# Optimization experiments

Hardware: AMD Instinct MI355X
Metric: run time of the kernel (lower is better)

## Reference

```python
import jax, jax.numpy as jnp
import numpy as np

N_NODES = 20000
N_ANCHORS = 64
D_IN = 128
D_OUT = 128
N_EDGES = N_NODES * N_ANCHORS  # 1,280,000


def setup_inputs() -> dict:
    key = jax.random.key(0)
    ks = jax.random.split(key, 8)
    feature = jax.random.normal(ks[0], (N_NODES, D_IN), dtype=jnp.float32)
    sp_dist = jax.random.uniform(ks[1], (N_EDGES,), dtype=jnp.float32)
    # xavier_uniform with relu gain ~ sqrt(2)*sqrt(6/(fan_in+fan_out))
    def xavier(k, fan_in, fan_out):
        bound = jnp.sqrt(2.0) * jnp.sqrt(6.0 / (fan_in + fan_out))
        return jax.random.uniform(k, (fan_in, fan_out), dtype=jnp.float32,
                                  minval=-bound, maxval=bound)
    Wu = xavier(ks[2], D_IN, D_OUT)
    Wv = xavier(ks[3], D_IN, D_OUT)
    Wpos = xavier(ks[4], D_OUT, 1)
    bu = jnp.zeros((D_OUT,), jnp.float32)
    bv = jnp.zeros((D_OUT,), jnp.float32)
    bpos = jnp.zeros((1,), jnp.float32)
    src = jax.random.randint(ks[5], (N_EDGES,), 0, N_NODES, dtype=jnp.int32)
    dst = jax.random.randint(ks[6], (N_EDGES,), 0, N_NODES, dtype=jnp.int32)
    anchor_eid = jax.random.randint(ks[7], (N_EDGES,), 0, N_EDGES, dtype=jnp.int32)
    return {"feature": feature, "sp_dist": sp_dist, "Wu": Wu, "bu": bu,
            "Wv": Wv, "bv": bv, "Wpos": Wpos, "bpos": bpos,
            "src": src, "dst": dst, "anchor_eid": anchor_eid}


def reference(feature, sp_dist, Wu, bu, Wv, bv, Wpos, bpos, src, dst, anchor_eid):
    # Dense projections of node features (linear_hidden_u / linear_hidden_v)
    u_feat = feature @ Wu + bu  # [N, D_OUT]
    v_feat = feature @ Wv + bv  # [N, D_OUT]
    # apply_edges u_mul_e + v_add_e, then index_select on anchor edges.
    # Gathering at anchor edges directly computes the same values as
    # computing all edge messages and then selecting the anchor subset.
    s = src[anchor_eid]            # [E]
    d = dst[anchor_eid]            # [E]
    sp = sp_dist[anchor_eid]       # [E]
    messages = u_feat[s] * sp[:, None] + v_feat[d]       # [E, D_OUT]
    messages = jax.nn.relu(messages).reshape(N_NODES, N_ANCHORS, D_OUT)
    out_position = (messages @ Wpos + bpos)[..., 0]      # [N, K]
    out_structure = messages.mean(axis=1)                # [N, D_OUT]
    return out_position, out_structure
```

## Files before the change

### kernel.cpp

```cpp
#include <hip/hip_runtime.h>

#define N_NODES   20000
#define N_ANCHORS 64
#define D         128
#define N_EDGES   (N_NODES * N_ANCHORS)
#define NCHUNK    4
#define CDIM      32

typedef float f32x4  __attribute__((ext_vector_type(4)));
typedef short bf16x8 __attribute__((ext_vector_type(8)));

static __device__ __forceinline__ unsigned short f32_to_bf16(float x) {
    unsigned int u = __float_as_uint(x);
    u += 0x7FFFu + ((u >> 16) & 1u);
    return (unsigned short)(u >> 16);
}
static __device__ __forceinline__ float bf_lo(unsigned int w) {
    return __uint_as_float(w << 16);
}
static __device__ __forceinline__ float bf_hi(unsigned int w) {
    return __uint_as_float(w & 0xFFFF0000u);
}

__global__ __launch_bounds__(256) void pack_kernel(
    const int* __restrict__ src, const int* __restrict__ dst,
    const float* __restrict__ sp_dist,
    unsigned long long* __restrict__ epack)
{
    const int e = blockIdx.x * 256 + threadIdx.x;
    const unsigned int s = (unsigned int)__builtin_nontemporal_load(&src[e]);
    const unsigned int d = (unsigned int)__builtin_nontemporal_load(&dst[e]);
    const float       sp = __builtin_nontemporal_load(&sp_dist[e]);
    epack[e] = (unsigned long long)(s | (d << 15)) |
               ((unsigned long long)__float_as_uint(sp) << 32);
}

__global__ __launch_bounds__(256) void meta_kernel(
    const unsigned long long* __restrict__ epack,
    const int* __restrict__ anchor_eid,
    unsigned long long* __restrict__ meta)
{
    const int e = blockIdx.x * 256 + threadIdx.x;
    const int eid = __builtin_nontemporal_load(&anchor_eid[e]);
    const unsigned long long m = epack[eid];
    __builtin_nontemporal_store(m, &meta[e]);
}

__global__ __launch_bounds__(256) void wcvt_kernel(
    const float* __restrict__ Wu, const float* __restrict__ Wv,
    unsigned short* __restrict__ Wt_u, unsigned short* __restrict__ Wt_v)
{
    const int t = blockIdx.x * 256 + threadIdx.x;
    const int k = t >> 7, j = t & 127;
    Wt_u[j * D + k] = f32_to_bf16(Wu[t]);
    Wt_v[j * D + k] = f32_to_bf16(Wv[t]);
}

__global__ __launch_bounds__(256) void proj_mfma_kernel(
    const float* __restrict__ feature,
    const unsigned short* __restrict__ Wt_u,
    const unsigned short* __restrict__ Wt_v,
    const float* __restrict__ bu, const float* __restrict__ bv,
    unsigned short* __restrict__ u_c, unsigned short* __restrict__ v_c)
{
    const int wave = threadIdx.x >> 6;
    const int lane = threadIdx.x & 63;
    const int n0   = blockIdx.x * 16;
    const int mat    = wave & 1;
    const int ctbase = (wave >> 1) * 4;

    const int row = lane & 15;
    const int kq  = lane >> 4;

    bf16x8 afrag[4];
    #pragma unroll
    for (int kt = 0; kt < 4; ++kt) {
        const float* fp = feature + (size_t)(n0 + row) * D + kt * 32 + kq * 8;
        const f32x4 f0 = *(const f32x4*)fp;
        const f32x4 f1 = *(const f32x4*)(fp + 4);
        bf16x8 a;
        #pragma unroll
        for (int e = 0; e < 4; ++e) a[e]     = (short)f32_to_bf16(f0[e]);
        #pragma unroll
        for (int e = 0; e < 4; ++e) a[4 + e] = (short)f32_to_bf16(f1[e]);
        afrag[kt] = a;
    }

    const unsigned short* Wt   = mat ? Wt_v : Wt_u;
    const float*          bias = mat ? bv   : bu;
    unsigned short*       outp = mat ? v_c  : u_c;

    #pragma unroll
    for (int t = 0; t < 4; ++t) {
        const int ct = ctbase + t;
        const int j  = ct * 16 + row;
        f32x4 acc = {0.f, 0.f, 0.f, 0.f};
        #pragma unroll
        for (int kt = 0; kt < 4; ++kt) {
            const bf16x8 b = *(const bf16x8*)(Wt + (size_t)j * D + kt * 32 + kq * 8);
            acc = __builtin_amdgcn_mfma_f32_16x16x32_bf16(afrag[kt], b, acc, 0, 0, 0);
        }
        const float bj  = bias[j];
        const int  cj   = ct >> 1;
        const int  dimc = (ct & 1) * 16 + row;
        #pragma unroll
        for (int r = 0; r < 4; ++r) {
            const int n = n0 + kq * 4 + r;
            outp[((size_t)cj * N_NODES + n) * CDIM + dimc] = f32_to_bf16(acc[r] + bj);
        }
    }
}

__global__ __launch_bounds__(256) void prefill_pos_kernel(
    const float* __restrict__ bpos, float* __restrict__ out_pos)
{
    const int i = blockIdx.x * 256 + threadIdx.x;
    const float bp = bpos[0];
    f32x4 v = {bp, bp, bp, bp};
    __builtin_nontemporal_store(v, (f32x4*)out_pos + i);
}

__global__ __launch_bounds__(256) void fused_chunk_kernel(
    const unsigned short* __restrict__ u_c, const unsigned short* __restrict__ v_c,
    const unsigned long long* __restrict__ meta,
    const float* __restrict__ Wpos,
    float* __restrict__ out_pos, float* __restrict__ out_struct)
{
    const int bid   = blockIdx.x;
    const int x     = bid & 7;
    const int chunk = x >> 1;
    const int half  = x & 1;
    const int nb    = bid >> 3;
    const int wave  = threadIdx.x >> 6;
    const int lane  = threadIdx.x & 63;
    const int n     = half * 10000 + nb * 4 + wave;

    const int sub = lane & 3;
    const int grp = lane >> 2;

    const unsigned long long mm =
        __builtin_nontemporal_load(&meta[(size_t)n * N_ANCHORS + lane]);
    const int   s  = (int)(mm & 0x7FFFu);
    const int   d  = (int)((mm >> 15) & 0x7FFFu);
    const float sp = __uint_as_float((unsigned int)(mm >> 32));

    const float4 wpA = ((const float4*)Wpos)[chunk * 8 + sub * 2];
    const float4 wpB = ((const float4*)Wpos)[chunk * 8 + sub * 2 + 1];

    const unsigned short* ub = u_c + (size_t)chunk * N_NODES * CDIM;
    const unsigned short* vb = v_c + (size_t)chunk * N_NODES * CDIM;

    float acc[8];
    #pragma unroll
    for (int k = 0; k < 8; ++k) acc[k] = 0.f;

    __shared__ float posbuf[4][N_ANCHORS];

    #pragma unroll
    for (int it = 0; it < 4; ++it) {
        const int a = it * 16 + grp;
        const int   sa  = __shfl(s,  a);
        const int   da  = __shfl(d,  a);
        const float spa = __shfl(sp, a);

        const uint4 uu = *(const uint4*)(ub + (size_t)sa * CDIM + sub * 8);
        const uint4 vv = *(const uint4*)(vb + (size_t)da * CDIM + sub * 8);

        float m[8];
        m[0] = fmaf(bf_lo(uu.x), spa, bf_lo(vv.x));
        m[1] = fmaf(bf_hi(uu.x), spa, bf_hi(vv.x));
        m[2] = fmaf(bf_lo(uu.y), spa, bf_lo(vv.y));
        m[3] = fmaf(bf_hi(uu.y), spa, bf_hi(vv.y));
        m[4] = fmaf(bf_lo(uu.z), spa, bf_lo(vv.z));
        m[5] = fmaf(bf_hi(uu.z), spa, bf_hi(vv.z));
        m[6] = fmaf(bf_lo(uu.w), spa, bf_lo(vv.w));
        m[7] = fmaf(bf_hi(uu.w), spa, bf_hi(vv.w));
        #pragma unroll
        for (int k = 0; k < 8; ++k) m[k] = fmaxf(m[k], 0.f);
        #pragma unroll
        for (int k = 0; k < 8; ++k) acc[k] += m[k];

        float p = m[0] * wpA.x + m[1] * wpA.y + m[2] * wpA.z + m[3] * wpA.w
                + m[4] * wpB.x + m[5] * wpB.y + m[6] * wpB.z + m[7] * wpB.w;
        p += __shfl_xor(p, 2);
        p += __shfl_xor(p, 1);
        if (sub == 0) posbuf[wave][a] = p;
    }

    #pragma unroll
    for (int k = 0; k < 8; ++k) {
        acc[k] += __shfl_xor(acc[k], 4);
        acc[k] += __shfl_xor(acc[k], 8);
        acc[k] += __shfl_xor(acc[k], 16);
        acc[k] += __shfl_xor(acc[k], 32);
    }

    __syncthreads();

    atomicAdd(&out_pos[(size_t)n * N_ANCHORS + lane], posbuf[wave][lane]);

    if (grp == 0) {
        const float inv = 1.0f / (float)N_ANCHORS;
        f32x4 o0, o1;
        o0.x = acc[0] * inv; o0.y = acc[1] * inv; o0.z = acc[2] * inv; o0.w = acc[3] * inv;
        o1.x = acc[4] * inv; o1.y = acc[5] * inv; o1.z = acc[6] * inv; o1.w = acc[7] * inv;
        float* os = out_struct + (size_t)n * D + chunk * CDIM + sub * 8;
        __builtin_nontemporal_store(o0, (f32x4*)os);
        __builtin_nontemporal_store(o1, (f32x4*)(os + 4));
    }
}

extern "C" void kernel_launch(void* const* d_in, const int* in_sizes, int n_in,
                              void* d_out, int out_size, void* d_ws, size_t ws_size,
                              hipStream_t stream) {
    const float* feature    = (const float*)d_in[0];
    const float* sp_dist    = (const float*)d_in[1];
    const float* Wu         = (const float*)d_in[2];
    const float* bu         = (const float*)d_in[3];
    const float* Wv         = (const float*)d_in[4];
    const float* bv         = (const float*)d_in[5];
    const float* Wpos       = (const float*)d_in[6];
    const float* bpos       = (const float*)d_in[7];
    const int*   src        = (const int*)d_in[8];
    const int*   dst        = (const int*)d_in[9];
    const int*   anchor_eid = (const int*)d_in[10];

    unsigned short* u_c = (unsigned short*)d_ws;
    unsigned short* v_c = u_c + (size_t)NCHUNK * N_NODES * CDIM;
    unsigned long long* epack = (unsigned long long*)d_ws;
    unsigned long long* meta =
        (unsigned long long*)((char*)d_ws + (size_t)2 * NCHUNK * N_NODES * CDIM * 2);

    float* out_pos    = (float*)d_out;
    float* out_struct = out_pos + (size_t)N_EDGES;

    unsigned short* Wt_u = (unsigned short*)out_struct;
    unsigned short* Wt_v = Wt_u + D * D;

    pack_kernel<<<N_EDGES / 256, 256, 0, stream>>>(src, dst, sp_dist, epack);
    meta_kernel<<<N_EDGES / 256, 256, 0, stream>>>(epack, anchor_eid, meta);
    wcvt_kernel<<<(D * D) / 256, 256, 0, stream>>>(Wu, Wv, Wt_u, Wt_v);
    proj_mfma_kernel<<<N_NODES / 16, 256, 0, stream>>>(feature, Wt_u, Wt_v,
                                                       bu, bv, u_c, v_c);
    prefill_pos_kernel<<<N_EDGES / 1024, 256, 0, stream>>>(bpos, out_pos);
    fused_chunk_kernel<<<N_NODES * NCHUNK / 4, 256, 0, stream>>>(
        u_c, v_c, meta, Wpos, out_pos, out_struct);
}
```

Measured before the change: 126.9 us.

## Merge pack, weight-convert and prefill kernels; use packed float2 math in fused kernel

```diff
diff --git a/kernel.cpp b/kernel.cpp
--- a/kernel.cpp
+++ b/kernel.cpp
@@ -7,6 +7,7 @@
 #define NCHUNK    4
 #define CDIM      32
 
+typedef float f32x2  __attribute__((ext_vector_type(2)));
 typedef float f32x4  __attribute__((ext_vector_type(4)));
 typedef short bf16x8 __attribute__((ext_vector_type(8)));
 
@@ -15,24 +16,44 @@
     u += 0x7FFFu + ((u >> 16) & 1u);
     return (unsigned short)(u >> 16);
 }
-static __device__ __forceinline__ float bf_lo(unsigned int w) {
-    return __uint_as_float(w << 16);
-}
-static __device__ __forceinline__ float bf_hi(unsigned int w) {
-    return __uint_as_float(w & 0xFFFF0000u);
-}
-
-__global__ __launch_bounds__(256) void pack_kernel(
+static __device__ __forceinline__ f32x2 bf2(unsigned int w) {
+    f32x2 r;
+    r.x = __uint_as_float(w << 16);
+    r.y = __uint_as_float(w & 0xFFFF0000u);
+    return r;
+}
+
+#define NB_PACK    (N_EDGES / 256)
+#define NB_WCVT    ((D * D) / 256)
+#define NB_PREFILL (N_EDGES / 1024)
+__global__ __launch_bounds__(256) void prep_kernel(
     const int* __restrict__ src, const int* __restrict__ dst,
     const float* __restrict__ sp_dist,
-    unsigned long long* __restrict__ epack)
-{
-    const int e = blockIdx.x * 256 + threadIdx.x;
-    const unsigned int s = (unsigned int)__builtin_nontemporal_load(&src[e]);
-    const unsigned int d = (unsigned int)__builtin_nontemporal_load(&dst[e]);
-    const float       sp = __builtin_nontemporal_load(&sp_dist[e]);
-    epack[e] = (unsigned long long)(s | (d << 15)) |
-               ((unsigned long long)__float_as_uint(sp) << 32);
+    const float* __restrict__ Wu, const float* __restrict__ Wv,
+    const float* __restrict__ bpos,
+    unsigned long long* __restrict__ epack,
+    unsigned short* __restrict__ Wt_u, unsigned short* __restrict__ Wt_v,
+    float* __restrict__ out_pos)
+{
+    const int bid = blockIdx.x;
+    if (bid < NB_PACK) {
+        const int e = bid * 256 + threadIdx.x;
+        const unsigned int s = (unsigned int)__builtin_nontemporal_load(&src[e]);
+        const unsigned int d = (unsigned int)__builtin_nontemporal_load(&dst[e]);
+        const float       sp = __builtin_nontemporal_load(&sp_dist[e]);
+        epack[e] = (unsigned long long)(s | (d << 15)) |
+                   ((unsigned long long)__float_as_uint(sp) << 32);
+    } else if (bid < NB_PACK + NB_WCVT) {
+        const int t = (bid - NB_PACK) * 256 + threadIdx.x;
+        const int k = t >> 7, j = t & 127;
+        Wt_u[j * D + k] = f32_to_bf16(Wu[t]);
+        Wt_v[j * D + k] = f32_to_bf16(Wv[t]);
+    } else {
+        const int i = (bid - NB_PACK - NB_WCVT) * 256 + threadIdx.x;
+        const float bp = bpos[0];
+        f32x4 v = {bp, bp, bp, bp};
+        __builtin_nontemporal_store(v, (f32x4*)out_pos + i);
+    }
 }
 
 __global__ __launch_bounds__(256) void meta_kernel(
@@ -44,16 +65,6 @@
     const int eid = __builtin_nontemporal_load(&anchor_eid[e]);
     const unsigned long long m = epack[eid];
     __builtin_nontemporal_store(m, &meta[e]);
-}
-
-__global__ __launch_bounds__(256) void wcvt_kernel(
-    const float* __restrict__ Wu, const float* __restrict__ Wv,
-    unsigned short* __restrict__ Wt_u, unsigned short* __restrict__ Wt_v)
-{
-    const int t = blockIdx.x * 256 + threadIdx.x;
-    const int k = t >> 7, j = t & 127;
-    Wt_u[j * D + k] = f32_to_bf16(Wu[t]);
-    Wt_v[j * D + k] = f32_to_bf16(Wv[t]);
 }
 
 __global__ __launch_bounds__(256) void proj_mfma_kernel(
@@ -109,15 +120,6 @@
             outp[((size_t)cj * N_NODES + n) * CDIM + dimc] = f32_to_bf16(acc[r] + bj);
         }
     }
-}
-
-__global__ __launch_bounds__(256) void prefill_pos_kernel(
-    const float* __restrict__ bpos, float* __restrict__ out_pos)
-{
-    const int i = blockIdx.x * 256 + threadIdx.x;
-    const float bp = bpos[0];
-    f32x4 v = {bp, bp, bp, bp};
-    __builtin_nontemporal_store(v, (f32x4*)out_pos + i);
 }
 
 __global__ __launch_bounds__(256) void fused_chunk_kernel(
@@ -144,15 +146,18 @@
     const int   d  = (int)((mm >> 15) & 0x7FFFu);
     const float sp = __uint_as_float((unsigned int)(mm >> 32));
 
-    const float4 wpA = ((const float4*)Wpos)[chunk * 8 + sub * 2];
-    const float4 wpB = ((const float4*)Wpos)[chunk * 8 + sub * 2 + 1];
+    f32x2 wp[4];
+    {
+        const f32x2* wpp = (const f32x2*)(Wpos + chunk * CDIM + sub * 8);
+        #pragma unroll
+        for (int q = 0; q < 4; ++q) wp[q] = wpp[q];
+    }
 
     const unsigned short* ub = u_c + (size_t)chunk * N_NODES * CDIM;
     const unsigned short* vb = v_c + (size_t)chunk * N_NODES * CDIM;
 
-    float acc[8];
-    #pragma unroll
-    for (int k = 0; k < 8; ++k) acc[k] = 0.f;
+    f32x2 acc0 = {0.f, 0.f}, acc1 = {0.f, 0.f}, acc2 = {0.f, 0.f}, acc3 = {0.f, 0.f};
+    const f32x2 zero2 = {0.f, 0.f};
 
     __shared__ float posbuf[4][N_ANCHORS];
 
@@ -166,27 +171,25 @@
         const uint4 uu = *(const uint4*)(ub + (size_t)sa * CDIM + sub * 8);
         const uint4 vv = *(const uint4*)(vb + (size_t)da * CDIM + sub * 8);
 
-        float m[8];
-        m[0] = fmaf(bf_lo(uu.x), spa, bf_lo(vv.x));
-        m[1] = fmaf(bf_hi(uu.x), spa, bf_hi(vv.x));
-        m[2] = fmaf(bf_lo(uu.y), spa, bf_lo(vv.y));
-        m[3] = fmaf(bf_hi(uu.y), spa, bf_hi(vv.y));
-        m[4] = fmaf(bf_lo(uu.z), spa, bf_lo(vv.z));
-        m[5] = fmaf(bf_hi(uu.z), spa, bf_hi(vv.z));
-        m[6] = fmaf(bf_lo(uu.w), spa, bf_lo(vv.w));
-        m[7] = fmaf(bf_hi(uu.w), spa, bf_hi(vv.w));
-        #pragma unroll
-        for (int k = 0; k < 8; ++k) m[k] = fmaxf(m[k], 0.f);
-        #pragma unroll
-        for (int k = 0; k < 8; ++k) acc[k] += m[k];
-
-        float p = m[0] * wpA.x + m[1] * wpA.y + m[2] * wpA.z + m[3] * wpA.w
-                + m[4] * wpB.x + m[5] * wpB.y + m[6] * wpB.z + m[7] * wpB.w;
+        f32x2 m0 = bf2(uu.x) * spa + bf2(vv.x);
+        f32x2 m1 = bf2(uu.y) * spa + bf2(vv.y);
+        f32x2 m2 = bf2(uu.z) * spa + bf2(vv.z);
+        f32x2 m3 = bf2(uu.w) * spa + bf2(vv.w);
+        m0 = __builtin_elementwise_max(m0, zero2);
+        m1 = __builtin_elementwise_max(m1, zero2);
+        m2 = __builtin_elementwise_max(m2, zero2);
+        m3 = __builtin_elementwise_max(m3, zero2);
+
+        acc0 += m0; acc1 += m1; acc2 += m2; acc3 += m3;
+
+        f32x2 pd = m0 * wp[0] + m1 * wp[1] + m2 * wp[2] + m3 * wp[3];
+        float p = pd.x + pd.y;
         p += __shfl_xor(p, 2);
         p += __shfl_xor(p, 1);
         if (sub == 0) posbuf[wave][a] = p;
     }
 
+    float acc[8] = {acc0.x, acc0.y, acc1.x, acc1.y, acc2.x, acc2.y, acc3.x, acc3.y};
     #pragma unroll
     for (int k = 0; k < 8; ++k) {
         acc[k] += __shfl_xor(acc[k], 4);
@@ -237,12 +240,11 @@
     unsigned short* Wt_u = (unsigned short*)out_struct;
     unsigned short* Wt_v = Wt_u + D * D;
 
-    pack_kernel<<<N_EDGES / 256, 256, 0, stream>>>(src, dst, sp_dist, epack);
+    prep_kernel<<<NB_PACK + NB_WCVT + NB_PREFILL, 256, 0, stream>>>(
+        src, dst, sp_dist, Wu, Wv, bpos, epack, Wt_u, Wt_v, out_pos);
     meta_kernel<<<N_EDGES / 256, 256, 0, stream>>>(epack, anchor_eid, meta);
-    wcvt_kernel<<<(D * D) / 256, 256, 0, stream>>>(Wu, Wv, Wt_u, Wt_v);
     proj_mfma_kernel<<<N_NODES / 16, 256, 0, stream>>>(feature, Wt_u, Wt_v,
                                                        bu, bv, u_c, v_c);
-    prefill_pos_kernel<<<N_EDGES / 1024, 256, 0, stream>>>(bpos, out_pos);
     fused_chunk_kernel<<<N_NODES * NCHUNK / 4, 256, 0, stream>>>(
         u_c, v_c, meta, Wpos, out_pos, out_struct);
 }
```

Result: faster. 123.8 us (-2.4%).
